# Optimization experiments

Measured on AMD Instinct MI355X. Metric: run time of the kernel, lower is better.

## Reference

```python
import jax, jax.numpy as jnp
import numpy as np

EPS = 1e-8


def setup_inputs() -> dict:
    key = jax.random.key(0)
    k1, k2, k3 = jax.random.split(key, 3)
    B, K, L, D = 4, 64, 128, 768
    context = jax.random.normal(k1, (B, K, 2, L, D), dtype=jnp.float32)
    # MlpModule(input_size=D): Linear(D, D) -> ReLU -> Linear(D, 1)
    w1 = jax.random.normal(k2, (D, D), dtype=jnp.float32) * (1.0 / np.sqrt(D))
    b1 = jnp.zeros((D,), dtype=jnp.float32)
    w2 = jax.random.normal(k3, (D, 1), dtype=jnp.float32) * (1.0 / np.sqrt(D))
    b2 = jnp.zeros((1,), dtype=jnp.float32)
    return {"context": context, "w1": w1, "b1": b1, "w2": w2, "b2": b2}


def reference(context, w1, b1, w2, b2):
    # context: [B, K, 2, L, D]; slice 0 = context tokens, slice 1 = entity tokens
    ctx = context[:, :, 0, :, :]   # [B, K, L, D]
    ent = context[:, :, 1, :, :]   # [B, K, L, D]

    ctx_norm = jnp.linalg.norm(ctx, axis=-1, keepdims=True)  # [B, K, L, 1]
    ent_norm = jnp.linalg.norm(ent, axis=-1, keepdims=True)  # [B, K, L, 1]

    # cosine-similarity score matrix: [B, K, L, L]
    denom = ctx_norm * jnp.swapaxes(ent_norm, -1, -2) + EPS
    scores = jnp.einsum('bkld,bkmd->bklm', ctx, ent) / denom

    # normalized embeddings (torch code does in-place /= before the stack)
    ctx_n = ctx / ctx_norm
    ent_n = ent / ent_norm

    # top-1 match along entity axis, gather matched entity token per context token
    argmax_idx = jnp.argmax(scores, axis=-1)                       # [B, K, L] int
    matched = jnp.take_along_axis(ent_n, argmax_idx[..., None], axis=2)  # [B, K, L, D]

    pair = jnp.stack([ctx_n, matched], axis=-2)  # [B, K, L, 2, D]

    # MLP: Linear(D,D) -> ReLU -> Linear(D,1), then sum over the pair axis
    h = jax.nn.relu(jnp.einsum('bklpd,de->bklpe', pair, w1) + b1)
    out = jnp.einsum('bklpd,do->bklpo', h, w2) + b2   # [B, K, L, 2, 1]
    out = jnp.sum(out, axis=-2)                        # [B, K, L, 1]
    return jnp.squeeze(out, axis=-1)                   # [B, K, L]
```

## Files before the change

kernel.cpp:

```cpp
#include <hip/hip_runtime.h>
#include <hip/hip_bf16.h>
#include <stdint.h>

#define NB 4
#define NK 64
#define NL 128
#define ND 768
#define NBK (NB*NK)
#define NROW (NBK*NL)
#define LD2 (NL*ND)
#define EPSF 1e-8f

typedef __bf16 bf16x8 __attribute__((ext_vector_type(8)));
typedef float  f32x4  __attribute__((ext_vector_type(4)));

__device__ __forceinline__ int row_off(int r) {
  if (r < NROW) return r*ND + (r >> 7)*LD2;
  int r2 = r - NROW;
  return r2*ND + (r2 >> 7)*LD2 + LD2;
}

__global__ void k0_w1t(const float* __restrict__ w1, __bf16* __restrict__ w1t) {
  int idx = blockIdx.x*256 + threadIdx.x;
  int e = idx % ND, k = idx / ND;
  float v = w1[k*ND + e];
  int g = (k >> 3) ^ (e & 7);
  w1t[e*ND + g*8 + (k & 7)] = (__bf16)v;
}

__global__ void k1_norms(const float* __restrict__ ctxall, float* __restrict__ norm) {
  int wave = threadIdx.x >> 6, lane = threadIdx.x & 63;
  int r = blockIdx.x*4 + wave;
  const f32x4* p = (const f32x4*)(ctxall + row_off(r));
  float acc = 0.f;
  #pragma unroll
  for (int i = 0; i < 3; i++) {
    f32x4 v = p[i*64 + lane];
    acc += v[0]*v[0] + v[1]*v[1] + v[2]*v[2] + v[3]*v[3];
  }
  #pragma unroll
  for (int m = 1; m < 64; m <<= 1) acc += __shfl_xor(acc, m);
  if (lane == 0) norm[r] = sqrtf(acc);
}

__global__ __launch_bounds__(512) void k2_scores(
    const float* __restrict__ ctxall, const float* __restrict__ norm,
    int* __restrict__ amax) {
  __shared__ float at[16][128];
  __shared__ float bt[16][128];
  int bk = blockIdx.x;
  const float* cbase = ctxall + bk*2*LD2;
  const float* ebase = cbase + LD2;
  int tid = threadIdx.x;
  int tr = tid >> 5, tc = tid & 31;
  float acc[8][4];
  #pragma unroll
  for (int j = 0; j < 8; j++)
    #pragma unroll
    for (int c = 0; c < 4; c++) acc[j][c] = 0.f;

  int srow = tid >> 2, skk = (tid & 3)*4;

  for (int k0 = 0; k0 < ND; k0 += 16) {
    f32x4 av = *(const f32x4*)(cbase + srow*ND + k0 + skk);
    f32x4 bv = *(const f32x4*)(ebase + srow*ND + k0 + skk);
    __syncthreads();
    #pragma unroll
    for (int j = 0; j < 4; j++) { at[skk+j][srow] = av[j]; bt[skk+j][srow] = bv[j]; }
    __syncthreads();
    #pragma unroll
    for (int kk = 0; kk < 16; kk++) {
      f32x4 a0 = *(const f32x4*)&at[kk][tr*8];
      f32x4 a1 = *(const f32x4*)&at[kk][tr*8 + 4];
      f32x4 b  = *(const f32x4*)&bt[kk][tc*4];
      #pragma unroll
      for (int j = 0; j < 4; j++)
        #pragma unroll
        for (int c = 0; c < 4; c++) {
          acc[j][c]   = fmaf(a0[j], b[c], acc[j][c]);
          acc[j+4][c] = fmaf(a1[j], b[c], acc[j+4][c]);
        }
    }
  }

  float en[4];
  #pragma unroll
  for (int c = 0; c < 4; c++) en[c] = norm[NROW + bk*NL + tc*4 + c];

  float bestv[8]; int besti[8];
  #pragma unroll
  for (int j = 0; j < 8; j++) {
    float cn = norm[bk*NL + tr*8 + j];
    bestv[j] = -3.0e38f; besti[j] = 0;
    #pragma unroll
    for (int c = 0; c < 4; c++) {
      float s = acc[j][c] / (cn*en[c] + EPSF);
      if (s > bestv[j]) { bestv[j] = s; besti[j] = tc*4 + c; }
    }
  }
  #pragma unroll
  for (int off = 1; off < 32; off <<= 1) {
    #pragma unroll
    for (int j = 0; j < 8; j++) {
      float ov = __shfl_xor(bestv[j], off);
      int   oi = __shfl_xor(besti[j], off);
      if (ov > bestv[j] || (ov == bestv[j] && oi < besti[j])) { bestv[j] = ov; besti[j] = oi; }
    }
  }
  if (tc == 0) {
    #pragma unroll
    for (int j = 0; j < 8; j++) amax[bk*NL + tr*8 + j] = besti[j];
  }
}

__global__ __launch_bounds__(256, 2) void k3_mlp(
    const float* __restrict__ ctxall, const float* __restrict__ norm,
    const __bf16* __restrict__ w1t, const float* __restrict__ b1,
    const float* __restrict__ w2, float* __restrict__ val) {
  __shared__ alignas(16) __bf16 btile[16*768];
  int tid = threadIdx.x;
  int wave = tid >> 6, lane = tid & 63;
  int quad = lane >> 4, eloc = lane & 15;
  int rbase = blockIdx.x*128 + wave*32;

  bf16x8 afrag[2][24];
  #pragma unroll
  for (int s = 0; s < 2; s++) {
    int r = rbase + s*16 + eloc;
    const float* src = ctxall + row_off(r);
    float rinv = 1.0f / norm[r];
    #pragma unroll
    for (int ks = 0; ks < 24; ks++) {
      const float* sp = src + ks*32 + quad*8;
      f32x4 v0 = *(const f32x4*)sp;
      f32x4 v1 = *(const f32x4*)(sp + 4);
      bf16x8 a;
      a[0] = (__bf16)(v0[0]*rinv); a[1] = (__bf16)(v0[1]*rinv);
      a[2] = (__bf16)(v0[2]*rinv); a[3] = (__bf16)(v0[3]*rinv);
      a[4] = (__bf16)(v1[0]*rinv); a[5] = (__bf16)(v1[1]*rinv);
      a[6] = (__bf16)(v1[2]*rinv); a[7] = (__bf16)(v1[3]*rinv);
      afrag[s][ks] = a;
    }
  }

  float oacc[2][4] = {{0,0,0,0},{0,0,0,0}};
  for (int nt = 0; nt < 48; nt++) {
    const __bf16* gsrc = w1t + nt*16*ND;
    __syncthreads();
    #pragma unroll
    for (int i = 0; i < 6; i++) {
      __builtin_amdgcn_global_load_lds(
        (const __attribute__((address_space(1))) unsigned int*)(gsrc + (i*256 + tid)*8),
        (__attribute__((address_space(3))) unsigned int*)(btile + (i*256 + tid)*8),
        16, 0, 0);
    }
    __syncthreads();

    f32x4 h0 = {0,0,0,0}, h1 = {0,0,0,0};
    #pragma unroll
    for (int ks = 0; ks < 24; ks++) {
      int g = ks*4 + quad;
      bf16x8 bfrag = *(const bf16x8*)(btile + eloc*ND + ((g ^ (eloc & 7))*8));
      h0 = __builtin_amdgcn_mfma_f32_16x16x32_bf16(afrag[0][ks], bfrag, h0, 0, 0, 0);
      h1 = __builtin_amdgcn_mfma_f32_16x16x32_bf16(afrag[1][ks], bfrag, h1, 0, 0, 0);
    }
    float b1v = b1[nt*16 + eloc];
    float w2v = w2[nt*16 + eloc];
    #pragma unroll
    for (int rr = 0; rr < 4; rr++) {
      oacc[0][rr] += fmaxf(h0[rr] + b1v, 0.f) * w2v;
      oacc[1][rr] += fmaxf(h1[rr] + b1v, 0.f) * w2v;
    }
  }
  #pragma unroll
  for (int m = 1; m < 16; m <<= 1)
    #pragma unroll
    for (int s = 0; s < 2; s++)
      #pragma unroll
      for (int rr = 0; rr < 4; rr++)
        oacc[s][rr] += __shfl_xor(oacc[s][rr], m);
  if (eloc == 0) {
    #pragma unroll
    for (int s = 0; s < 2; s++)
      #pragma unroll
      for (int rr = 0; rr < 4; rr++)
        val[rbase + s*16 + quad*4 + rr] = oacc[s][rr];
  }
}

__global__ void k4_out(const float* __restrict__ val, const int* __restrict__ amax,
                       const float* __restrict__ b2, float* __restrict__ out) {
  int i = blockIdx.x*256 + threadIdx.x;
  int bk = i >> 7;
  out[i] = val[i] + val[NROW + bk*NL + amax[i]] + 2.0f*b2[0];
}

extern "C" void kernel_launch(void* const* d_in, const int* in_sizes, int n_in,
                              void* d_out, int out_size, void* d_ws, size_t ws_size,
                              hipStream_t stream) {
  const float* ctxall = (const float*)d_in[0];
  const float* w1 = (const float*)d_in[1];
  const float* b1 = (const float*)d_in[2];
  const float* w2 = (const float*)d_in[3];
  const float* b2 = (const float*)d_in[4];
  float* out = (float*)d_out;

  char* ws = (char*)d_ws;
  float* norm = (float*)ws;
  int*   amax = (int*)(ws + 262144);
  float* val  = (float*)(ws + 262144 + 131072);
  __bf16* w1t = (__bf16*)(ws + 655360);

  hipLaunchKernelGGL(k0_w1t,   dim3(ND*ND/256), dim3(256), 0, stream, w1, w1t);
  hipLaunchKernelGGL(k1_norms, dim3(2*NROW/4),  dim3(256), 0, stream, ctxall, norm);
  hipLaunchKernelGGL(k2_scores,dim3(NBK),       dim3(512), 0, stream, ctxall, norm, amax);
  hipLaunchKernelGGL(k3_mlp,   dim3(2*NROW/128),dim3(256), 0, stream, ctxall, norm, w1t, b1, w2, val);
  hipLaunchKernelGGL(k4_out,   dim3(NROW/256),  dim3(256), 0, stream, val, amax, b2, out);
}
```

Measured before the change: 475.6 us.

## Fuse row norms into score kernel, double-buffer tiles, and tile the W1 transpose

Removes the separate norm kernel by accumulating squared sums inside the score GEMM while tiles are staged, so the norms come from LDS. The score kernel now splits each batch into two halves of 64 context rows, which doubles the block count, and uses double-buffered padded shared tiles with register prefetch so there is one barrier per k-step. The W1 transpose/convert kernel now goes through an LDS tile and does coalesced vector stores. As a trade-off, the entity tiles are loaded twice per batch (once per half), and the norm reductions add extra barriers.

```diff
diff --git a/kernel.cpp b/kernel.cpp
--- a/kernel.cpp
+++ b/kernel.cpp
@@ -20,59 +20,77 @@
   return r2*ND + (r2 >> 7)*LD2 + LD2;
 }
 
-__global__ void k0_w1t(const float* __restrict__ w1, __bf16* __restrict__ w1t) {
-  int idx = blockIdx.x*256 + threadIdx.x;
-  int e = idx % ND, k = idx / ND;
-  float v = w1[k*ND + e];
-  int g = (k >> 3) ^ (e & 7);
-  w1t[e*ND + g*8 + (k & 7)] = (__bf16)v;
-}
-
-__global__ void k1_norms(const float* __restrict__ ctxall, float* __restrict__ norm) {
-  int wave = threadIdx.x >> 6, lane = threadIdx.x & 63;
-  int r = blockIdx.x*4 + wave;
-  const f32x4* p = (const f32x4*)(ctxall + row_off(r));
-  float acc = 0.f;
-  #pragma unroll
-  for (int i = 0; i < 3; i++) {
-    f32x4 v = p[i*64 + lane];
-    acc += v[0]*v[0] + v[1]*v[1] + v[2]*v[2] + v[3]*v[3];
-  }
-  #pragma unroll
-  for (int m = 1; m < 64; m <<= 1) acc += __shfl_xor(acc, m);
-  if (lane == 0) norm[r] = sqrtf(acc);
-}
-
-__global__ __launch_bounds__(512) void k2_scores(
-    const float* __restrict__ ctxall, const float* __restrict__ norm,
+__global__ __launch_bounds__(256) void k0_w1t(const float* __restrict__ w1,
+                                              __bf16* __restrict__ w1t) {
+  __shared__ float tile[64][68];
+  int kb = (blockIdx.x / 12) * 64, eb = (blockIdx.x % 12) * 64;
+  int t = threadIdx.x;
+  int r = t >> 2, c0 = (t & 3) * 16;
+  #pragma unroll
+  for (int j = 0; j < 4; j++) {
+    f32x4 v = *(const f32x4*)(w1 + (kb + r)*ND + eb + c0 + j*4);
+    *(f32x4*)&tile[r][c0 + j*4] = v;
+  }
+  __syncthreads();
+  int e = t & 63, gi = t >> 6;
+  int eg = eb + e;
+  #pragma unroll
+  for (int g2 = 0; g2 < 2; g2++) {
+    int g = gi*2 + g2;
+    bf16x8 o;
+    #pragma unroll
+    for (int j = 0; j < 8; j++) o[j] = (__bf16)tile[g*8 + j][e];
+    int G = (kb >> 3) + (g ^ (eg & 7));
+    *(bf16x8*)(w1t + eg*ND + G*8) = o;
+  }
+}
+
+__global__ __launch_bounds__(256) void k2_scores(
+    const float* __restrict__ ctxall, float* __restrict__ norm,
     int* __restrict__ amax) {
-  __shared__ float at[16][128];
-  __shared__ float bt[16][128];
-  int bk = blockIdx.x;
-  const float* cbase = ctxall + bk*2*LD2;
-  const float* ebase = cbase + LD2;
+  __shared__ float at[2][16][68];
+  __shared__ float bt[2][16][132];
+  __shared__ float red[256];
+  __shared__ float cnorm[64], enorm[128];
+  int bk = blockIdx.x >> 1, half = blockIdx.x & 1;
+  const float* cbase = ctxall + bk*2*LD2 + half*64*ND;
+  const float* ebase = ctxall + bk*2*LD2 + LD2;
   int tid = threadIdx.x;
   int tr = tid >> 5, tc = tid & 31;
+  int ar = tid >> 2, ak = (tid & 3)*4;
+  int br = tid >> 1, bkk = (tid & 1)*8;
+
   float acc[8][4];
   #pragma unroll
   for (int j = 0; j < 8; j++)
     #pragma unroll
     for (int c = 0; c < 4; c++) acc[j][c] = 0.f;
-
-  int srow = tid >> 2, skk = (tid & 3)*4;
-
-  for (int k0 = 0; k0 < ND; k0 += 16) {
-    f32x4 av = *(const f32x4*)(cbase + srow*ND + k0 + skk);
-    f32x4 bv = *(const f32x4*)(ebase + srow*ND + k0 + skk);
+  float sqa = 0.f, sqb = 0.f;
+
+  f32x4 av  = *(const f32x4*)(cbase + ar*ND + ak);
+  f32x4 bv0 = *(const f32x4*)(ebase + br*ND + bkk);
+  f32x4 bv1 = *(const f32x4*)(ebase + br*ND + bkk + 4);
+
+  int p = 0;
+  for (int t = 0; t < 48; t++) {
+    #pragma unroll
+    for (int j = 0; j < 4; j++) { at[p][ak+j][ar] = av[j];     sqa += av[j]*av[j]; }
+    #pragma unroll
+    for (int j = 0; j < 4; j++) { bt[p][bkk+j][br] = bv0[j];   sqb += bv0[j]*bv0[j]; }
+    #pragma unroll
+    for (int j = 0; j < 4; j++) { bt[p][bkk+4+j][br] = bv1[j]; sqb += bv1[j]*bv1[j]; }
     __syncthreads();
-    #pragma unroll
-    for (int j = 0; j < 4; j++) { at[skk+j][srow] = av[j]; bt[skk+j][srow] = bv[j]; }
-    __syncthreads();
+    if (t < 47) {
+      int k0 = (t+1)*16;
+      av  = *(const f32x4*)(cbase + ar*ND + k0 + ak);
+      bv0 = *(const f32x4*)(ebase + br*ND + k0 + bkk);
+      bv1 = *(const f32x4*)(ebase + br*ND + k0 + bkk + 4);
+    }
     #pragma unroll
     for (int kk = 0; kk < 16; kk++) {
-      f32x4 a0 = *(const f32x4*)&at[kk][tr*8];
-      f32x4 a1 = *(const f32x4*)&at[kk][tr*8 + 4];
-      f32x4 b  = *(const f32x4*)&bt[kk][tc*4];
+      f32x4 a0 = *(const f32x4*)&at[p][kk][tr*8];
+      f32x4 a1 = *(const f32x4*)&at[p][kk][tr*8 + 4];
+      f32x4 b  = *(const f32x4*)&bt[p][kk][tc*4];
       #pragma unroll
       for (int j = 0; j < 4; j++)
         #pragma unroll
@@ -81,16 +99,34 @@
           acc[j+4][c] = fmaf(a1[j], b[c], acc[j+4][c]);
         }
     }
-  }
+    p ^= 1;
+  }
+
+  red[tid] = sqa; __syncthreads();
+  if (tid < 64) {
+    float s = red[tid*4] + red[tid*4+1] + red[tid*4+2] + red[tid*4+3];
+    float n = sqrtf(s);
+    cnorm[tid] = n;
+    norm[bk*NL + half*64 + tid] = n;
+  }
+  __syncthreads();
+  red[tid] = sqb; __syncthreads();
+  if (tid < 128) {
+    float s = red[tid*2] + red[tid*2+1];
+    float n = sqrtf(s);
+    enorm[tid] = n;
+    if (half == 0) norm[NROW + bk*NL + tid] = n;
+  }
+  __syncthreads();
 
   float en[4];
   #pragma unroll
-  for (int c = 0; c < 4; c++) en[c] = norm[NROW + bk*NL + tc*4 + c];
+  for (int c = 0; c < 4; c++) en[c] = enorm[tc*4 + c];
 
   float bestv[8]; int besti[8];
   #pragma unroll
   for (int j = 0; j < 8; j++) {
-    float cn = norm[bk*NL + tr*8 + j];
+    float cn = cnorm[tr*8 + j];
     bestv[j] = -3.0e38f; besti[j] = 0;
     #pragma unroll
     for (int c = 0; c < 4; c++) {
@@ -109,7 +145,7 @@
   }
   if (tc == 0) {
     #pragma unroll
-    for (int j = 0; j < 8; j++) amax[bk*NL + tr*8 + j] = besti[j];
+    for (int j = 0; j < 8; j++) amax[bk*NL + half*64 + tr*8 + j] = besti[j];
   }
 }
 
@@ -211,9 +247,8 @@
   float* val  = (float*)(ws + 262144 + 131072);
   __bf16* w1t = (__bf16*)(ws + 655360);
 
-  hipLaunchKernelGGL(k0_w1t,   dim3(ND*ND/256), dim3(256), 0, stream, w1, w1t);
-  hipLaunchKernelGGL(k1_norms, dim3(2*NROW/4),  dim3(256), 0, stream, ctxall, norm);
-  hipLaunchKernelGGL(k2_scores,dim3(NBK),       dim3(512), 0, stream, ctxall, norm, amax);
-  hipLaunchKernelGGL(k3_mlp,   dim3(2*NROW/128),dim3(256), 0, stream, ctxall, norm, w1t, b1, w2, val);
-  hipLaunchKernelGGL(k4_out,   dim3(NROW/256),  dim3(256), 0, stream, val, amax, b2, out);
-}
+  hipLaunchKernelGGL(k0_w1t,   dim3(144),         dim3(256), 0, stream, w1, w1t);
+  hipLaunchKernelGGL(k2_scores,dim3(2*NBK),       dim3(256), 0, stream, ctxall, norm, amax);
+  hipLaunchKernelGGL(k3_mlp,   dim3(2*NROW/128),  dim3(256), 0, stream, ctxall, norm, w1t, b1, w2, val);
+  hipLaunchKernelGGL(k4_out,   dim3(NROW/256),    dim3(256), 0, stream, val, amax, b2, out);
+}
```

After: 424.2 us. -10.8%, faster.
